# Optimization experiments

Measured on AMD Instinct MI355X. Metric: run time of the kernel, lower is better.

Reference implementation:

```python
import jax, jax.numpy as jnp
import numpy as np

MU_P = 0.15
MASK_ID = 103
VOCAB = 30522


def setup_inputs() -> dict:
    key = jax.random.key(0)
    k1, k2 = jax.random.split(key)
    B, C, S = 1024, 4, 2048
    # first half = per-token sampling weights, second half = shared_tokens (unused by the math)
    my_attention_mask = jax.random.uniform(k1, (B, C, 2 * S), dtype=jnp.float32)
    attention_mask = jnp.ones((B, C, S), dtype=jnp.int32)  # tokenizer attention mask
    input_ids = jax.random.randint(k2, (B, C, S), 0, VOCAB, dtype=jnp.int32)
    return {"my_attention_mask": my_attention_mask,
            "attention_mask": attention_mask,
            "input_ids": input_ids}


def reference(my_attention_mask, attention_mask, input_ids):
    """Weighted sampling WITHOUT replacement per (batch, choice) row via Gumbel-top-k.

    Original loops over (k, j), draws num_to_mask = floor(sum(tok_mask) * N(mu_p, sigma))
    indices from the nonzero weights in my_attention_mask[..., :S] (prob ~ weight),
    masks those token positions in input_ids and emits the indicator mask.
    Gumbel-top-k: keys = log(w) + Gumbel noise; the top-num_to_mask keys are a
    weighted sample without replacement from w. Zero-weight positions get -inf keys.
    """
    B, C, S = input_ids.shape
    w = my_attention_mask[..., :S]  # [B, C, S] sampling weights

    key = jax.random.key(42)
    kg, kn = jax.random.split(key)
    sigma = min(0.05, MU_P / 4.0)
    frac = MU_P + sigma * jax.random.normal(kn, (B, C), dtype=jnp.float32)
    num_to_mask = jnp.floor(
        attention_mask.sum(axis=-1).astype(jnp.float32) * frac
    ).astype(jnp.int32)  # [B, C]

    log_w = jnp.where(w > 0, jnp.log(jnp.maximum(w, 1e-30)), -jnp.inf)
    keys = log_w + jax.random.gumbel(kg, w.shape, dtype=jnp.float32)  # [B, C, S]

    # rank[i] = position of i in descending key order (double argsort)
    order = jnp.argsort(-keys, axis=-1)
    rank = jnp.argsort(order, axis=-1)
    new_attention_mask = (rank < num_to_mask[..., None]).astype(jnp.int32)  # [B, C, S]

    new_input_ids = jnp.where(new_attention_mask == 1, MASK_ID, input_ids)
    discriminator_labels = -new_attention_mask
    return new_input_ids, new_attention_mask, discriminator_labels
```

## Files before the change

### kernel.cpp

```cpp
#include <hip/hip_runtime.h>
#include <stdint.h>
#include <math.h>

#define SLEN 2048
#define EPT 8
#define NTHREADS 256
#define TOKENS_PER_OUT 8388608

__host__ __device__ __forceinline__ void tf2x32(uint32_t k0, uint32_t k1,
                                                uint32_t x0, uint32_t x1,
                                                uint32_t &o0, uint32_t &o1) {
  uint32_t ks2 = 0x1BD11BDAu ^ k0 ^ k1;
  x0 += k0; x1 += k1;
#define TFR(r) { x0 += x1; x1 = (x1 << (r)) | (x1 >> (32 - (r))); x1 ^= x0; }
  TFR(13) TFR(15) TFR(26) TFR(6)
  x0 += k1;  x1 += ks2 + 1u;
  TFR(17) TFR(29) TFR(16) TFR(24)
  x0 += ks2; x1 += k0 + 2u;
  TFR(13) TFR(15) TFR(26) TFR(6)
  x0 += k0;  x1 += k1 + 3u;
  TFR(17) TFR(29) TFR(16) TFR(24)
  x0 += k1;  x1 += ks2 + 4u;
  TFR(13) TFR(15) TFR(26) TFR(6)
  x0 += ks2; x1 += k0 + 5u;
#undef TFR
  o0 = x0; o1 = x1;
}

__device__ __forceinline__ void tf4_bits(uint32_t k0, uint32_t k1,
                                         uint32_t cbase, uint32_t bits[4]) {
  const uint32_t ks2 = 0x1BD11BDAu ^ k0 ^ k1;
  uint32_t x0[4], x1[4];
#pragma unroll
  for (int i = 0; i < 4; ++i) { x0[i] = k0; x1[i] = (cbase + (uint32_t)i) + k1; }
#define TFR4(r)                                                         \
  _Pragma("unroll")                                                     \
  for (int i = 0; i < 4; ++i) {                                         \
    x0[i] += x1[i];                                                     \
    x1[i] = (x1[i] << (r)) | (x1[i] >> (32 - (r)));                     \
    x1[i] ^= x0[i];                                                     \
  }                                                                     \
  __builtin_amdgcn_sched_barrier(0);
#define INJ4(a, b)                                                      \
  _Pragma("unroll")                                                     \
  for (int i = 0; i < 4; ++i) { x0[i] += (a); x1[i] += (b); }
  TFR4(13) TFR4(15) TFR4(26) TFR4(6)
  INJ4(k1, ks2 + 1u)
  TFR4(17) TFR4(29) TFR4(16) TFR4(24)
  INJ4(ks2, k0 + 2u)
  TFR4(13) TFR4(15) TFR4(26) TFR4(6)
  INJ4(k0, k1 + 3u)
  TFR4(17) TFR4(29) TFR4(16) TFR4(24)
  INJ4(k1, ks2 + 4u)
  TFR4(13) TFR4(15) TFR4(26) TFR4(6)
  INJ4(ks2, k0 + 5u)
#undef TFR4
#undef INJ4
#pragma unroll
  for (int i = 0; i < 4; ++i) bits[i] = x0[i] ^ x1[i];
}

__device__ __forceinline__ float u01_from_bits(uint32_t bits) {
  return __uint_as_float((bits >> 9) | 0x3F800000u) - 1.0f;
}

#define SBAR() __builtin_amdgcn_sched_barrier(0)

__device__ __forceinline__ void log8_cr(const float x[8], float out[8]) {
#pragma clang fp contract(off)
  double m[8]; int e[8];
#pragma unroll
  for (int i = 0; i < 8; ++i) {
    uint32_t xb   = __float_as_uint(x[i]);
    uint32_t mant = xb & 0x7FFFFFu;
    int      ee   = (int)(xb >> 23) - 127;
    bool     big  = mant > 0x3504F3u;
    e[i] = ee + (big ? 1 : 0);
    uint32_t hi = (big ? 0x3FE00000u : 0x3FF00000u) | (mant >> 3);
    uint32_t lo = mant << 29;
    m[i] = __longlong_as_double(((long long)hi << 32) | (long long)lo);
  }
  SBAR();
  double mp1[8];
#pragma unroll
  for (int i = 0; i < 8; ++i) mp1[i] = m[i] + 1.0;
  SBAR();
  double y[8];
#pragma unroll
  for (int i = 0; i < 8; ++i) y[i] = __builtin_amdgcn_rcp(mp1[i]);
  SBAR();
#pragma unroll
  for (int i = 0; i < 8; ++i) y[i] = fma(fma(-mp1[i], y[i], 1.0), y[i], y[i]);
  SBAR();
  double r[8];
#pragma unroll
  for (int i = 0; i < 8; ++i) r[i] = (m[i] - 1.0) * y[i];
  SBAR();
  double t[8];
#pragma unroll
  for (int i = 0; i < 8; ++i) t[i] = r[i] * r[i];
  SBAR();
  double p[8];
#pragma unroll
  for (int i = 0; i < 8; ++i) p[i] = fma(0.07692307692307693, t[i], 0.09090909090909091);
  SBAR();
#pragma unroll
  for (int i = 0; i < 8; ++i) p[i] = fma(p[i], t[i], 0.1111111111111111);
  SBAR();
#pragma unroll
  for (int i = 0; i < 8; ++i) p[i] = fma(p[i], t[i], 0.14285714285714285);
  SBAR();
#pragma unroll
  for (int i = 0; i < 8; ++i) p[i] = fma(p[i], t[i], 0.2);
  SBAR();
#pragma unroll
  for (int i = 0; i < 8; ++i) p[i] = fma(p[i], t[i], 0.3333333333333333);
  SBAR();
#pragma unroll
  for (int i = 0; i < 8; ++i) p[i] = fma(p[i], t[i], 1.0);
  SBAR();
#pragma unroll
  for (int i = 0; i < 8; ++i) r[i] = r[i] + r[i];
  SBAR();
#pragma unroll
  for (int i = 0; i < 8; ++i) p[i] = r[i] * p[i];
  SBAR();
#pragma unroll
  for (int i = 0; i < 8; ++i)
    out[i] = (float)fma((double)e[i], 0.6931471805599453, p[i]);
}

__device__ __forceinline__ float log_cr(float x) {
#pragma clang fp contract(off)
  uint32_t xb   = __float_as_uint(x);
  uint32_t mant = xb & 0x7FFFFFu;
  int      e    = (int)(xb >> 23) - 127;
  bool     big  = mant > 0x3504F3u;
  e += big ? 1 : 0;
  uint32_t hi = (big ? 0x3FE00000u : 0x3FF00000u) | (mant >> 3);
  double m = __longlong_as_double(((long long)hi << 32) | (long long)(mant << 29));
  double mp1 = m + 1.0;
  double y = __builtin_amdgcn_rcp(mp1);
  y = fma(fma(-mp1, y, 1.0), y, y);
  double r = (m - 1.0) * y;
  double t = r * r;
  double p = fma(0.07692307692307693, t, 0.09090909090909091);
  p = fma(p, t, 0.1111111111111111);
  p = fma(p, t, 0.14285714285714285);
  p = fma(p, t, 0.2);
  p = fma(p, t, 0.3333333333333333);
  p = fma(p, t, 1.0);
  return (float)fma((double)e, 0.6931471805599453, (r + r) * p);
}

__device__ float erfinv_xla(float x) {
#pragma clang fp contract(off)
  float x2  = x * x;
  float nx2 = -x2;
  float l1p;
  if (fabsf(nx2) < 1e-4f) {
    l1p = (-0.5f * nx2 + 1.0f) * nx2;
  } else {
    l1p = log_cr(1.0f + nx2);
  }
  float w = -l1p;
  float p;
  if (w < 5.0f) {
    float ww = w - 2.5f;
    p = 2.81022636e-08f;
    p = p * ww + 3.43273939e-07f;
    p = p * ww + -3.5233877e-06f;
    p = p * ww + -4.39150654e-06f;
    p = p * ww + 0.00021858087f;
    p = p * ww + -0.00125372503f;
    p = p * ww + -0.00417768164f;
    p = p * ww + 0.246640727f;
    p = p * ww + 1.50140941f;
  } else {
    float ww = sqrtf(w) - 3.0f;
    p = -0.000200214257f;
    p = p * ww + 0.000100950558f;
    p = p * ww + 0.00134934322f;
    p = p * ww + -0.00367342844f;
    p = p * ww + 0.00573950773f;
    p = p * ww + -0.0076224613f;
    p = p * ww + 0.00943887047f;
    p = p * ww + 1.00167406f;
    p = p * ww + 2.83297682f;
  }
  return p * x;
}

__global__ __launch_bounds__(NTHREADS, 8)
void gumbel_topk_mask(const float* __restrict__ wfull,
                      const int*   __restrict__ attn,
                      const int*   __restrict__ ids,
                      int* __restrict__ out,
                      uint32_t kg0, uint32_t kg1, uint32_t kn0, uint32_t kn1) {
#pragma clang fp contract(off)
  const int row  = blockIdx.x;
  const int t    = threadIdx.x;
  const int lane = t & 63;
  const int wid  = t >> 6;

  __shared__ __align__(16) uint32_t hist[2][256];
  __shared__ uint32_t wsum[4];
  __shared__ uint32_t prefix_s;
  __shared__ uint32_t remaining_s;
  __shared__ int      done_s;

  const size_t rbase = (size_t)row * SLEN;
  const size_t wbase = (size_t)row * (2 * SLEN);
  const int    base  = t * EPT;

  hist[0][t] = 0u;
  hist[1][t] = 0u;

  const float4* wv4 = (const float4*)(wfull + wbase + base);
  float4 w0 = wv4[0], w1 = wv4[1];
  const int4* av4 = (const int4*)(attn + rbase + base);
  int4 a0 = av4[0], a1 = av4[1];
  int psum = a0.x + a0.y + a0.z + a0.w + a1.x + a1.y + a1.z + a1.w;

  uint32_t bits[EPT];
  tf4_bits(kg0, kg1, (uint32_t)(rbase + base + 0), bits + 0);
  tf4_bits(kg0, kg1, (uint32_t)(rbase + base + 4), bits + 4);
  SBAR();

  float wl[EPT] = {w0.x, w0.y, w0.z, w0.w, w1.x, w1.y, w1.z, w1.w};
  float uu[EPT];
#pragma unroll
  for (int e = 0; e < EPT; ++e) {
    float f = u01_from_bits(bits[e]);
    uu[e] = fmaxf(1.17549435e-38f, f * 1.0f + 1.17549435e-38f);
  }
  SBAR();
  float l1[EPT];
  log8_cr(uu, l1);
  float wm[EPT];
#pragma unroll
  for (int e = 0; e < EPT; ++e) wm[e] = fmaxf(wl[e], 1e-30f);
  float lw[EPT];
  log8_cr(wm, lw);
  float nl1[EPT];
#pragma unroll
  for (int e = 0; e < EPT; ++e) nl1[e] = -l1[e];
  float l2[EPT];
  log8_cr(nl1, l2);
  SBAR();
  uint32_t mloc[EPT];
#pragma unroll
  for (int e = 0; e < EPT; ++e) {
    float key = (wl[e] > 0.0f) ? (lw[e] + (-l2[e])) : -__builtin_inff();
    uint32_t kb = __float_as_uint(key);
    mloc[e] = (kb & 0x80000000u) ? ~kb : (kb | 0x80000000u);
  }

  const int4* iv4 = (const int4*)(ids + rbase + base);
  int4 i0 = iv4[0], i1 = iv4[1];

#pragma unroll
  for (int off = 32; off; off >>= 1) psum += __shfl_down(psum, off, 64);
  if (lane == 0) wsum[wid] = (uint32_t)psum;
  if (t == 0) { prefix_s = 0u; done_s = 0; }
  __syncthreads();

#pragma unroll
  for (int e = 0; e < EPT; ++e) atomicAdd(&hist[0][mloc[e] >> 24], 1u);

  int cur = 0;
  for (int p = 3; p >= 0; --p) {
    __syncthreads();
    if (t < 64) {
      uint32_t need = 0u;
      if (p == 3) {
        int asum = (int)(wsum[0] + wsum[1] + wsum[2] + wsum[3]);
        uint32_t o0, o1;
        tf2x32(kn0, kn1, 0u, (uint32_t)row, o0, o1);
        float f   = u01_from_bits(o0 ^ o1);
        float lo  = __uint_as_float(0xBF7FFFFFu);
        float u2  = fmaxf(lo, f * 2.0f + lo);
        float z   = erfinv_xla(u2);
        float nrm = 1.4142135623730951f * z;
        float frac = 0.15f + 0.0375f * nrm;
        int kk = (int)floorf((float)asum * frac);
        if (kk <= 0)         { if (t == 0) { prefix_s = 0xFFFFFFFFu; remaining_s = 0u;   done_s = 1; } }
        else if (kk >= SLEN) { if (t == 0) { prefix_s = 0u;          remaining_s = SLEN; done_s = 1; } }
        else need = (uint32_t)kk;
      } else {
        need = remaining_s;
      }
      if (need) {
        uint4 hq = ((const uint4*)hist[cur])[t];
        uint32_t gs  = hq.x + hq.y + hq.z + hq.w;
        uint32_t sfx = gs;
#pragma unroll
        for (int off = 1; off < 64; off <<= 1) {
          uint32_t n = __shfl_down(sfx, off, 64);
          if (t + off < 64) sfx += n;
        }
        uint32_t Gex = sfx - gs;
        uint32_t S3 = Gex;
        uint32_t S2 = S3 + hq.w;
        uint32_t S1 = S2 + hq.z;
        uint32_t S0 = S1 + hq.y;
        uint32_t hh[4] = {hq.x, hq.y, hq.z, hq.w};
        uint32_t SS[4] = {S0, S1, S2, S3};
#pragma unroll
        for (int i = 0; i < 4; ++i) {
          if (hh[i] && SS[i] < need && need <= SS[i] + hh[i]) {
            prefix_s |= ((uint32_t)(4 * t + i)) << (8 * p);
            uint32_t rem = need - SS[i];
            remaining_s = rem;
            if (rem == hh[i]) done_s = 1;
          }
        }
      }
    } else {
      int idx = t - 64;
      hist[cur ^ 1][idx] = 0u;
      if (idx < 64) hist[cur ^ 1][idx + 192] = 0u;
    }
    __syncthreads();
    if (done_s) break;
    if (p > 0) {
      uint32_t pref = prefix_s;
      int sh = 8 * p;
#pragma unroll
      for (int e = 0; e < EPT; ++e) {
        uint32_t m = mloc[e];
        if ((m >> sh) == (pref >> sh))
          atomicAdd(&hist[cur ^ 1][(m >> (sh - 8)) & 255u], 1u);
      }
    }
    cur ^= 1;
  }
  uint32_t T = prefix_s;
  uint32_t r = remaining_s;

  int local_eq = 0;
#pragma unroll
  for (int e = 0; e < EPT; ++e) local_eq += (mloc[e] == T) ? 1 : 0;
  uint32_t v = (uint32_t)local_eq;
#pragma unroll
  for (int off = 1; off < 64; off <<= 1) {
    uint32_t n = __shfl_up(v, off, 64);
    if (lane >= off) v += n;
  }
  if (lane == 63) wsum[wid] = v;
  __syncthreads();
  uint32_t add = 0;
  for (int i = 0; i < wid; ++i) add += wsum[i];
  uint32_t excl = add + v - (uint32_t)local_eq;

  int idv[EPT] = {i0.x, i0.y, i0.z, i0.w, i1.x, i1.y, i1.z, i1.w};
  int oid[EPT], omk[EPT], olb[EPT];
#pragma unroll
  for (int e = 0; e < EPT; ++e) {
    uint32_t m = mloc[e];
    bool eq  = (m == T);
    bool msk = (m > T) || (eq && (excl < r));
    excl += eq ? 1u : 0u;
    oid[e] = msk ? 103 : idv[e];
    omk[e] = msk ? 1 : 0;
    olb[e] = msk ? -1 : 0;
  }
  int4* po = (int4*)(out + rbase + base);
  po[0] = make_int4(oid[0], oid[1], oid[2], oid[3]);
  po[1] = make_int4(oid[4], oid[5], oid[6], oid[7]);
  int4* pm = (int4*)(out + TOKENS_PER_OUT + rbase + base);
  pm[0] = make_int4(omk[0], omk[1], omk[2], omk[3]);
  pm[1] = make_int4(omk[4], omk[5], omk[6], omk[7]);
  int4* pl = (int4*)(out + 2 * TOKENS_PER_OUT + rbase + base);
  pl[0] = make_int4(olb[0], olb[1], olb[2], olb[3]);
  pl[1] = make_int4(olb[4], olb[5], olb[6], olb[7]);
}

extern "C" void kernel_launch(void* const* d_in, const int* in_sizes, int n_in,
                              void* d_out, int out_size, void* d_ws, size_t ws_size,
                              hipStream_t stream) {
  (void)n_in; (void)d_ws; (void)ws_size; (void)out_size;
  const float* wfull = (const float*)d_in[0];
  const int*   attn  = (const int*)d_in[1];
  const int*   ids   = (const int*)d_in[2];
  int* out = (int*)d_out;

  uint32_t kg0, kg1, kn0, kn1, o0, o1;
  tf2x32(0u, 42u, 0u, 0u, o0, o1); kg0 = o0; kg1 = o1;
  tf2x32(0u, 42u, 0u, 1u, o0, o1); kn0 = o0; kn1 = o1;

  int rows = in_sizes[1] / SLEN;
  hipLaunchKernelGGL(gumbel_topk_mask, dim3(rows), dim3(NTHREADS), 0, stream,
                     wfull, attn, ids, out, kg0, kg1, kn0, kn1);
}
```

Before: 202.7 us.

## Process one row per wavefront to drop block-wide barriers in radix select

Each row moves from a whole 256-thread block to a single 64-lane wavefront: four rows per block, 32 elements per lane. The radix-select histogram passes now use per-wave LDS histograms with wave barriers and ballot/shuffle broadcasts in place of __syncthreads and shared scalars. The per-row sample count is computed redundantly by every lane up front. The aim is to remove block-level synchronisation and serial single-wave phases, at the cost of higher register pressure (32 keys per lane), lower occupancy bounds, and more LDS atomic contention per wave.

```diff
diff --git a/kernel.cpp b/kernel.cpp
--- a/kernel.cpp
+++ b/kernel.cpp
@@ -3,8 +3,9 @@
 #include <math.h>
 
 #define SLEN 2048
-#define EPT 8
+#define EPT 32
 #define NTHREADS 256
+#define ROWS_PER_BLOCK 4
 #define TOKENS_PER_OUT 8388608
 
 __host__ __device__ __forceinline__ void tf2x32(uint32_t k0, uint32_t k1,
@@ -191,152 +192,143 @@
   return p * x;
 }
 
-__global__ __launch_bounds__(NTHREADS, 8)
+__global__ __launch_bounds__(NTHREADS, 4)
 void gumbel_topk_mask(const float* __restrict__ wfull,
                       const int*   __restrict__ attn,
                       const int*   __restrict__ ids,
                       int* __restrict__ out,
                       uint32_t kg0, uint32_t kg1, uint32_t kn0, uint32_t kn1) {
 #pragma clang fp contract(off)
-  const int row  = blockIdx.x;
   const int t    = threadIdx.x;
   const int lane = t & 63;
   const int wid  = t >> 6;
-
-  __shared__ __align__(16) uint32_t hist[2][256];
-  __shared__ uint32_t wsum[4];
-  __shared__ uint32_t prefix_s;
-  __shared__ uint32_t remaining_s;
-  __shared__ int      done_s;
+  const int row  = blockIdx.x * ROWS_PER_BLOCK + wid;
+
+  __shared__ __align__(16) uint32_t hist[ROWS_PER_BLOCK][256];
 
   const size_t rbase = (size_t)row * SLEN;
   const size_t wbase = (size_t)row * (2 * SLEN);
-  const int    base  = t * EPT;
-
-  hist[0][t] = 0u;
-  hist[1][t] = 0u;
-
+  const int    base  = lane * EPT;
+
+  ((uint4*)hist[wid])[lane] = make_uint4(0u, 0u, 0u, 0u);
+
+  const int4* av4 = (const int4*)(attn + rbase + base);
+  int psum = 0;
+#pragma unroll
+  for (int c = 0; c < 8; ++c) {
+    int4 a = av4[c];
+    psum += a.x + a.y + a.z + a.w;
+  }
+#pragma unroll
+  for (int off = 32; off; off >>= 1) psum += __shfl_down(psum, off, 64);
+  int asum = __shfl(psum, 0, 64);
+
+  uint32_t no0, no1;
+  tf2x32(kn0, kn1, 0u, (uint32_t)row, no0, no1);
+  float f0  = u01_from_bits(no0 ^ no1);
+  float lo  = __uint_as_float(0xBF7FFFFFu);
+  float u2  = fmaxf(lo, f0 * 2.0f + lo);
+  float z   = erfinv_xla(u2);
+  float nrm = 1.4142135623730951f * z;
+  float frac = 0.15f + 0.0375f * nrm;
+  int kk = (int)floorf((float)asum * frac);
+
+  uint32_t mloc[EPT];
   const float4* wv4 = (const float4*)(wfull + wbase + base);
-  float4 w0 = wv4[0], w1 = wv4[1];
-  const int4* av4 = (const int4*)(attn + rbase + base);
-  int4 a0 = av4[0], a1 = av4[1];
-  int psum = a0.x + a0.y + a0.z + a0.w + a1.x + a1.y + a1.z + a1.w;
-
-  uint32_t bits[EPT];
-  tf4_bits(kg0, kg1, (uint32_t)(rbase + base + 0), bits + 0);
-  tf4_bits(kg0, kg1, (uint32_t)(rbase + base + 4), bits + 4);
-  SBAR();
-
-  float wl[EPT] = {w0.x, w0.y, w0.z, w0.w, w1.x, w1.y, w1.z, w1.w};
-  float uu[EPT];
-#pragma unroll
-  for (int e = 0; e < EPT; ++e) {
-    float f = u01_from_bits(bits[e]);
-    uu[e] = fmaxf(1.17549435e-38f, f * 1.0f + 1.17549435e-38f);
-  }
-  SBAR();
-  float l1[EPT];
-  log8_cr(uu, l1);
-  float wm[EPT];
-#pragma unroll
-  for (int e = 0; e < EPT; ++e) wm[e] = fmaxf(wl[e], 1e-30f);
-  float lw[EPT];
-  log8_cr(wm, lw);
-  float nl1[EPT];
-#pragma unroll
-  for (int e = 0; e < EPT; ++e) nl1[e] = -l1[e];
-  float l2[EPT];
-  log8_cr(nl1, l2);
-  SBAR();
-  uint32_t mloc[EPT];
-#pragma unroll
-  for (int e = 0; e < EPT; ++e) {
-    float key = (wl[e] > 0.0f) ? (lw[e] + (-l2[e])) : -__builtin_inff();
-    uint32_t kb = __float_as_uint(key);
-    mloc[e] = (kb & 0x80000000u) ? ~kb : (kb | 0x80000000u);
-  }
-
-  const int4* iv4 = (const int4*)(ids + rbase + base);
-  int4 i0 = iv4[0], i1 = iv4[1];
-
-#pragma unroll
-  for (int off = 32; off; off >>= 1) psum += __shfl_down(psum, off, 64);
-  if (lane == 0) wsum[wid] = (uint32_t)psum;
-  if (t == 0) { prefix_s = 0u; done_s = 0; }
-  __syncthreads();
-
-#pragma unroll
-  for (int e = 0; e < EPT; ++e) atomicAdd(&hist[0][mloc[e] >> 24], 1u);
-
-  int cur = 0;
-  for (int p = 3; p >= 0; --p) {
-    __syncthreads();
-    if (t < 64) {
-      uint32_t need = 0u;
-      if (p == 3) {
-        int asum = (int)(wsum[0] + wsum[1] + wsum[2] + wsum[3]);
-        uint32_t o0, o1;
-        tf2x32(kn0, kn1, 0u, (uint32_t)row, o0, o1);
-        float f   = u01_from_bits(o0 ^ o1);
-        float lo  = __uint_as_float(0xBF7FFFFFu);
-        float u2  = fmaxf(lo, f * 2.0f + lo);
-        float z   = erfinv_xla(u2);
-        float nrm = 1.4142135623730951f * z;
-        float frac = 0.15f + 0.0375f * nrm;
-        int kk = (int)floorf((float)asum * frac);
-        if (kk <= 0)         { if (t == 0) { prefix_s = 0xFFFFFFFFu; remaining_s = 0u;   done_s = 1; } }
-        else if (kk >= SLEN) { if (t == 0) { prefix_s = 0u;          remaining_s = SLEN; done_s = 1; } }
-        else need = (uint32_t)kk;
-      } else {
-        need = remaining_s;
+#pragma unroll
+  for (int c = 0; c < 4; ++c) {
+    float4 w0 = wv4[2 * c + 0], w1 = wv4[2 * c + 1];
+    uint32_t bits[8];
+    tf4_bits(kg0, kg1, (uint32_t)(rbase + base + 8 * c + 0), bits + 0);
+    tf4_bits(kg0, kg1, (uint32_t)(rbase + base + 8 * c + 4), bits + 4);
+    SBAR();
+    float wl[8] = {w0.x, w0.y, w0.z, w0.w, w1.x, w1.y, w1.z, w1.w};
+    float uu[8];
+#pragma unroll
+    for (int e = 0; e < 8; ++e) {
+      float f = u01_from_bits(bits[e]);
+      uu[e] = fmaxf(1.17549435e-38f, f * 1.0f + 1.17549435e-38f);
+    }
+    SBAR();
+    float l1[8];
+    log8_cr(uu, l1);
+    float wm[8];
+#pragma unroll
+    for (int e = 0; e < 8; ++e) wm[e] = fmaxf(wl[e], 1e-30f);
+    float lw[8];
+    log8_cr(wm, lw);
+    float nl1[8];
+#pragma unroll
+    for (int e = 0; e < 8; ++e) nl1[e] = -l1[e];
+    float l2[8];
+    log8_cr(nl1, l2);
+    SBAR();
+#pragma unroll
+    for (int e = 0; e < 8; ++e) {
+      float key = (wl[e] > 0.0f) ? (lw[e] + (-l2[e])) : -__builtin_inff();
+      uint32_t kb = __float_as_uint(key);
+      mloc[8 * c + e] = (kb & 0x80000000u) ? ~kb : (kb | 0x80000000u);
+    }
+  }
+
+  uint32_t T, r;
+  if (kk <= 0)          { T = 0xFFFFFFFFu; r = 0u; }
+  else if (kk >= SLEN)  { T = 0u;          r = (uint32_t)SLEN; }
+  else {
+    T = 0u;
+    uint32_t need = (uint32_t)kk;
+    asm volatile("s_waitcnt lgkmcnt(0)" ::: "memory");
+#pragma unroll
+    for (int e = 0; e < EPT; ++e)
+      atomicAdd(&hist[wid][mloc[e] >> 24], 1u);
+    for (int p = 3; ; --p) {
+      asm volatile("s_waitcnt lgkmcnt(0)" ::: "memory");
+      __builtin_amdgcn_wave_barrier();
+      uint4 hq = ((const uint4*)hist[wid])[lane];
+      uint32_t gs  = hq.x + hq.y + hq.z + hq.w;
+      uint32_t sfx = gs;
+#pragma unroll
+      for (int off = 1; off < 64; off <<= 1) {
+        uint32_t n = __shfl_down(sfx, off, 64);
+        if (lane + off < 64) sfx += n;
       }
-      if (need) {
-        uint4 hq = ((const uint4*)hist[cur])[t];
-        uint32_t gs  = hq.x + hq.y + hq.z + hq.w;
-        uint32_t sfx = gs;
-#pragma unroll
-        for (int off = 1; off < 64; off <<= 1) {
-          uint32_t n = __shfl_down(sfx, off, 64);
-          if (t + off < 64) sfx += n;
-        }
-        uint32_t Gex = sfx - gs;
-        uint32_t S3 = Gex;
-        uint32_t S2 = S3 + hq.w;
-        uint32_t S1 = S2 + hq.z;
-        uint32_t S0 = S1 + hq.y;
-        uint32_t hh[4] = {hq.x, hq.y, hq.z, hq.w};
-        uint32_t SS[4] = {S0, S1, S2, S3};
-#pragma unroll
-        for (int i = 0; i < 4; ++i) {
-          if (hh[i] && SS[i] < need && need <= SS[i] + hh[i]) {
-            prefix_s |= ((uint32_t)(4 * t + i)) << (8 * p);
-            uint32_t rem = need - SS[i];
-            remaining_s = rem;
-            if (rem == hh[i]) done_s = 1;
-          }
+      uint32_t Gex = sfx - gs;
+      uint32_t S3 = Gex;
+      uint32_t S2 = S3 + hq.w;
+      uint32_t S1 = S2 + hq.z;
+      uint32_t S0 = S1 + hq.y;
+      uint32_t hh[4] = {hq.x, hq.y, hq.z, hq.w};
+      uint32_t SS[4] = {S0, S1, S2, S3};
+      int haswin = 0; uint32_t binv = 0u, remv = 0u; int donev = 0;
+#pragma unroll
+      for (int i = 0; i < 4; ++i) {
+        if (hh[i] && SS[i] < need && need <= SS[i] + hh[i]) {
+          haswin = 1;
+          binv = (uint32_t)(4 * lane + i);
+          remv = need - SS[i];
+          donev = (remv == hh[i]) ? 1 : 0;
         }
       }
-    } else {
-      int idx = t - 64;
-      hist[cur ^ 1][idx] = 0u;
-      if (idx < 64) hist[cur ^ 1][idx + 192] = 0u;
-    }
-    __syncthreads();
-    if (done_s) break;
-    if (p > 0) {
-      uint32_t pref = prefix_s;
-      int sh = 8 * p;
+      unsigned long long wmask = __ballot(haswin);
+      int src = (int)(__ffsll((unsigned long long)wmask) - 1);
+      uint32_t bin = (uint32_t)__shfl((int)binv, src, 64);
+      uint32_t rem = (uint32_t)__shfl((int)remv, src, 64);
+      int     done = __shfl(donev, src, 64);
+      T |= bin << (8 * p);
+      need = rem;
+      if (done || p == 0) { r = rem; break; }
+      ((uint4*)hist[wid])[lane] = make_uint4(0u, 0u, 0u, 0u);
+      asm volatile("s_waitcnt lgkmcnt(0)" ::: "memory");
+      __builtin_amdgcn_wave_barrier();
+      const int sh = 8 * p;
 #pragma unroll
       for (int e = 0; e < EPT; ++e) {
         uint32_t m = mloc[e];
-        if ((m >> sh) == (pref >> sh))
-          atomicAdd(&hist[cur ^ 1][(m >> (sh - 8)) & 255u], 1u);
+        if ((m >> sh) == (T >> sh))
+          atomicAdd(&hist[wid][(m >> (sh - 8)) & 255u], 1u);
       }
     }
-    cur ^= 1;
-  }
-  uint32_t T = prefix_s;
-  uint32_t r = remaining_s;
+  }
 
   int local_eq = 0;
 #pragma unroll
@@ -347,33 +339,34 @@
     uint32_t n = __shfl_up(v, off, 64);
     if (lane >= off) v += n;
   }
-  if (lane == 63) wsum[wid] = v;
-  __syncthreads();
-  uint32_t add = 0;
-  for (int i = 0; i < wid; ++i) add += wsum[i];
-  uint32_t excl = add + v - (uint32_t)local_eq;
-
-  int idv[EPT] = {i0.x, i0.y, i0.z, i0.w, i1.x, i1.y, i1.z, i1.w};
-  int oid[EPT], omk[EPT], olb[EPT];
-#pragma unroll
-  for (int e = 0; e < EPT; ++e) {
-    uint32_t m = mloc[e];
-    bool eq  = (m == T);
-    bool msk = (m > T) || (eq && (excl < r));
-    excl += eq ? 1u : 0u;
-    oid[e] = msk ? 103 : idv[e];
-    omk[e] = msk ? 1 : 0;
-    olb[e] = msk ? -1 : 0;
-  }
+  uint32_t excl = v - (uint32_t)local_eq;
+
+  const int4* iv4 = (const int4*)(ids + rbase + base);
   int4* po = (int4*)(out + rbase + base);
-  po[0] = make_int4(oid[0], oid[1], oid[2], oid[3]);
-  po[1] = make_int4(oid[4], oid[5], oid[6], oid[7]);
   int4* pm = (int4*)(out + TOKENS_PER_OUT + rbase + base);
-  pm[0] = make_int4(omk[0], omk[1], omk[2], omk[3]);
-  pm[1] = make_int4(omk[4], omk[5], omk[6], omk[7]);
   int4* pl = (int4*)(out + 2 * TOKENS_PER_OUT + rbase + base);
-  pl[0] = make_int4(olb[0], olb[1], olb[2], olb[3]);
-  pl[1] = make_int4(olb[4], olb[5], olb[6], olb[7]);
+#pragma unroll
+  for (int c = 0; c < 4; ++c) {
+    int4 i0 = iv4[2 * c + 0], i1 = iv4[2 * c + 1];
+    int idv[8] = {i0.x, i0.y, i0.z, i0.w, i1.x, i1.y, i1.z, i1.w};
+    int oid[8], omk[8], olb[8];
+#pragma unroll
+    for (int e = 0; e < 8; ++e) {
+      uint32_t m = mloc[8 * c + e];
+      bool eq  = (m == T);
+      bool msk = (m > T) || (eq && (excl < r));
+      excl += eq ? 1u : 0u;
+      oid[e] = msk ? 103 : idv[e];
+      omk[e] = msk ? 1 : 0;
+      olb[e] = msk ? -1 : 0;
+    }
+    po[2 * c + 0] = make_int4(oid[0], oid[1], oid[2], oid[3]);
+    po[2 * c + 1] = make_int4(oid[4], oid[5], oid[6], oid[7]);
+    pm[2 * c + 0] = make_int4(omk[0], omk[1], omk[2], omk[3]);
+    pm[2 * c + 1] = make_int4(omk[4], omk[5], omk[6], omk[7]);
+    pl[2 * c + 0] = make_int4(olb[0], olb[1], olb[2], olb[3]);
+    pl[2 * c + 1] = make_int4(olb[4], olb[5], olb[6], olb[7]);
+  }
 }
 
 extern "C" void kernel_launch(void* const* d_in, const int* in_sizes, int n_in,
@@ -390,6 +383,6 @@
   tf2x32(0u, 42u, 0u, 1u, o0, o1); kn0 = o0; kn1 = o1;
 
   int rows = in_sizes[1] / SLEN;
-  hipLaunchKernelGGL(gumbel_topk_mask, dim3(rows), dim3(NTHREADS), 0, stream,
-                     wfull, attn, ids, out, kg0, kg1, kn0, kn1);
-}
+  hipLaunchKernelGGL(gumbel_topk_mask, dim3(rows / ROWS_PER_BLOCK), dim3(NTHREADS),
+                     0, stream, wfull, attn, ids, out, kg0, kg1, kn0, kn1);
+}
```

Result: slower. 271.5 us (+33.9%).
